# Kernel tuning notes

Hardware: AMD Instinct MI355X
Metric: run time of the kernel (lower is better)

## Reference

```python
import jax, jax.numpy as jnp
import numpy as np

NUM_EXPERTS = 8
TOP_K = 2
DIM = 1024
HIDDEN = 4096
BATCH, SEQ = 16, 32


def setup_inputs() -> dict:
    key = jax.random.key(0)
    k1, k2, k3, k4, k5 = jax.random.split(key, 5)
    scale = 1.0 / np.sqrt(DIM)
    return {
        "hidden_states": jax.random.normal(k1, (BATCH, SEQ, DIM), dtype=jnp.float32),
        "gate_w": jax.random.normal(k2, (NUM_EXPERTS, DIM), dtype=jnp.float32) * scale,
        "w1": jax.random.normal(k3, (NUM_EXPERTS, HIDDEN, DIM), dtype=jnp.float32) * scale,
        "w3": jax.random.normal(k4, (NUM_EXPERTS, HIDDEN, DIM), dtype=jnp.float32) * scale,
        "w2": jax.random.normal(k5, (NUM_EXPERTS, DIM, HIDDEN), dtype=jnp.float32) * (1.0 / np.sqrt(HIDDEN)),
    }


def reference(hidden_states, gate_w, w1, w3, w2):
    B, S, D = hidden_states.shape
    x = hidden_states.reshape(-1, D)  # [T, D]

    # Router: softmax in fp32, top-k, renormalize (Mixtral style)
    router_logits = x @ gate_w.T  # [T, E]
    probs = jax.nn.softmax(router_logits.astype(jnp.float32), axis=-1)
    routing_weights, selected_experts = jax.lax.top_k(probs, TOP_K)  # [T, K]
    routing_weights = routing_weights / routing_weights.sum(axis=-1, keepdims=True)
    routing_weights = routing_weights.astype(x.dtype)

    # Per-token per-expert combine coefficient: coef[t, e] = sum_k w[t,k] * 1[sel[t,k]==e]
    coef = (jax.nn.one_hot(selected_experts, NUM_EXPERTS, dtype=x.dtype)
            * routing_weights[..., None]).sum(axis=1)  # [T, E]

    # SwiGLU FFN for all experts (grouped GEMM form), combined by coef.
    h1 = jnp.einsum('td,ehd->teh', x, w1)           # [T, E, H]
    h3 = jnp.einsum('td,ehd->teh', x, w3)           # [T, E, H]
    act = jax.nn.silu(h1) * h3                      # [T, E, H]
    expert_out = jnp.einsum('teh,edh->ted', act, w2)  # [T, E, D]
    out = jnp.einsum('ted,te->td', expert_out, coef)  # [T, D]
    return out.reshape(B, S, D)
```

## Files before the change

kernel.cpp:

```cpp
#include <hip/hip_runtime.h>
#include <hip/hip_bf16.h>

#define E_ 8
#define D_ 1024
#define H_ 4096
#define T_ 512
#define A_ 1024
#define BM_ 192
#define NBUF 3

typedef __attribute__((ext_vector_type(8))) short bf16x8;
typedef __attribute__((ext_vector_type(4))) float f32x4;

__device__ __forceinline__ unsigned short f2bf(float f) {
  __hip_bfloat16 h = __float2bfloat16(f);
  return *reinterpret_cast<unsigned short*>(&h);
}

__device__ __forceinline__ bf16x8 pk8(float4 a, float4 b) {
  bf16x8 r;
  r[0] = (short)f2bf(a.x); r[1] = (short)f2bf(a.y);
  r[2] = (short)f2bf(a.z); r[3] = (short)f2bf(a.w);
  r[4] = (short)f2bf(b.x); r[5] = (short)f2bf(b.y);
  r[6] = (short)f2bf(b.z); r[7] = (short)f2bf(b.w);
  return r;
}

__device__ __forceinline__ void gl16(const void* g, void* l) {
  __builtin_amdgcn_global_load_lds(
      (const __attribute__((address_space(1))) unsigned int*)g,
      (__attribute__((address_space(3))) unsigned int*)l, 16, 0, 0);
}

__global__ void moe_router(const float* __restrict__ x,
                           const float* __restrict__ gw,
                           unsigned short* __restrict__ xb,
                           int* __restrict__ sel,
                           float* __restrict__ wtop) {
  const int t = blockIdx.x;
  const int lane = threadIdx.x;
  const float* xr = x + (size_t)t * D_;

  float4 xv[4];
#pragma unroll
  for (int i = 0; i < 4; ++i) xv[i] = *reinterpret_cast<const float4*>(xr + (i * 64 + lane) * 4);
#pragma unroll
  for (int i = 0; i < 4; ++i) {
    ushort4 u;
    u.x = f2bf(xv[i].x); u.y = f2bf(xv[i].y); u.z = f2bf(xv[i].z); u.w = f2bf(xv[i].w);
    *reinterpret_cast<ushort4*>(xb + (size_t)t * D_ + (i * 64 + lane) * 4) = u;
  }

  float lg[E_];
  for (int e = 0; e < E_; ++e) {
    const float* g = gw + (size_t)e * D_;
    float p = 0.f;
#pragma unroll
    for (int i = 0; i < 4; ++i) {
      float4 gv = *reinterpret_cast<const float4*>(g + (i * 64 + lane) * 4);
      p += xv[i].x * gv.x + xv[i].y * gv.y + xv[i].z * gv.z + xv[i].w * gv.w;
    }
#pragma unroll
    for (int off = 32; off; off >>= 1) p += __shfl_xor(p, off);
    lg[e] = p;
  }
  if (lane == 0) {
    float m = lg[0];
    for (int e = 1; e < E_; ++e) m = fmaxf(m, lg[e]);
    float pr[E_];
    float s = 0.f;
    for (int e = 0; e < E_; ++e) { pr[e] = __expf(lg[e] - m); s += pr[e]; }
    const float inv = 1.f / s;
    for (int e = 0; e < E_; ++e) pr[e] *= inv;
    float v0 = -1.f, v1 = -1.f; int i0 = 0, i1 = 0;
    for (int e = 0; e < E_; ++e) {
      float p = pr[e];
      if (p > v0)      { v1 = v0; i1 = i0; v0 = p; i0 = e; }
      else if (p > v1) { v1 = p; i1 = e; }
    }
    const float s2 = 1.f / (v0 + v1);
    sel[2 * t] = i0; sel[2 * t + 1] = i1;
    wtop[2 * t] = v0 * s2; wtop[2 * t + 1] = v1 * s2;
  }
}

__global__ void moe_compact(const int* __restrict__ sel,
                            const float* __restrict__ wtop,
                            int* __restrict__ counts,
                            int* __restrict__ offsets,
                            int* __restrict__ tok,
                            int* __restrict__ slotof,
                            float* __restrict__ coef) {
  const int tid = threadIdx.x;
  const int e = tid >> 6;
  const int lane = tid & 63;
  __shared__ int cnt[E_], offs[E_];

  int base = 0;
  for (int c = 0; c < T_ / 64; ++c) {
    const int t = c * 64 + lane;
    const bool f = (sel[2 * t] == e) || (sel[2 * t + 1] == e);
    base += __popcll(__ballot(f));
  }
  if (lane == 0) cnt[e] = base;
  __syncthreads();
  if (tid == 0) {
    int o = 0;
    for (int i = 0; i < E_; ++i) { offs[i] = o; o += cnt[i]; }
  }
  __syncthreads();
  if (lane == 0) { counts[e] = cnt[e]; offsets[e] = offs[e]; }

  int pos = offs[e];
  for (int c = 0; c < T_ / 64; ++c) {
    const int t = c * 64 + lane;
    const int s0 = sel[2 * t], s1 = sel[2 * t + 1];
    const bool f = (s0 == e) || (s1 == e);
    unsigned long long b = __ballot(f);
    const int myp = pos + __popcll(b & ((1ull << lane) - 1ull));
    if (f) {
      const int k = (s0 == e) ? 0 : 1;
      tok[myp] = t;
      slotof[2 * t + k] = myp;
      coef[myp] = wtop[2 * t + k];
    }
    pos += __popcll(b);
  }
}


#define WAITS(it, nit)                                                        \
    if ((it) == 0)              asm volatile("s_waitcnt vmcnt(4)" ::: "memory"); \
    else if ((it) == (nit) - 1) asm volatile("s_waitcnt vmcnt(3)" ::: "memory"); \
    else                        asm volatile("s_waitcnt vmcnt(7)" ::: "memory"); \
    __builtin_amdgcn_s_barrier();                                             \
    __builtin_amdgcn_sched_barrier(0);

#define STAGE1(s, kt) do {                                                    \
    gl16(b1src[0] + (kt), &B1s[s][wid * 256]);                                \
    gl16(b1src[1] + (kt), &B1s[s][1024 + wid * 256]);                         \
    gl16(b3src[0] + (kt), &B3s[s][wid * 256]);                                \
    gl16(b3src[1] + (kt), &B3s[s][1024 + wid * 256]);                         \
  } while (0)

__launch_bounds__(256, 3)
__global__ void moe_ffn1(const unsigned short* __restrict__ xb,
                         const float* __restrict__ w1,
                         const float* __restrict__ w3,
                         const int* __restrict__ counts,
                         const int* __restrict__ offsets,
                         const int* __restrict__ tok,
                         unsigned short* __restrict__ act) {
  const int bid = blockIdx.x;
  const int e = bid & 7;
  const int hg = bid >> 3;
  const int count = counts[e];
  const int off = offsets[e];
  const int hbase = hg * 64;

  __shared__ float B1s[NBUF][64 * 32];
  __shared__ float B3s[NBUF][64 * 32];

  const int tid = threadIdx.x;
  const int lane = tid & 63, wid = tid >> 6;
  const int lr = lane & 15, kg = lane >> 4;
  const int wm = wid * 48;

  const int cB = (((lane & 7) ^ (lane >> 3)) << 2);
  const float* b1src[2];
  const float* b3src[2];
#pragma unroll
  for (int j = 0; j < 2; ++j) {
    const int row = (j * 4 + wid) * 8 + (lane >> 3);
    b1src[j] = w1 + ((size_t)e * H_ + hbase + row) * D_ + cB;
    b3src[j] = w3 + ((size_t)e * H_ + hbase + row) * D_ + cB;
  }
  const int q0 = (((2 * kg) ^ (lr & 7)) << 2);
  const int q1 = (((2 * kg + 1) ^ (lr & 7)) << 2);

  for (int m0 = 0; m0 < count; m0 += BM_) {
    const unsigned short* ap[3];
#pragma unroll
    for (int mf = 0; mf < 3; ++mf) {
      const int row = m0 + wm + mf * 16 + lr;
      const int cr = (row < count) ? row : (count - 1);
      ap[mf] = xb + (size_t)tok[off + cr] * D_ + kg * 8;
    }
    const int qq = count - m0 - wm;
    const int mfn = (qq <= 0) ? 0 : ((qq + 15) >> 4 < 3 ? (qq + 15) >> 4 : 3);

    f32x4 acc1[3][4] = {};
    f32x4 acc3[3][4] = {};

    STAGE1(0, 0);
    STAGE1(1, 32);

    int cur = 0;
    for (int it = 0; it < 32; ++it) {
      WAITS(it, 32);

      bf16x8 af[3];
#pragma unroll
      for (int mf = 0; mf < 3; ++mf)
        af[mf] = *reinterpret_cast<const bf16x8*>(ap[mf] + it * 32);

      if (it + 2 < 32) {
        int s2 = cur + 2; if (s2 >= NBUF) s2 -= NBUF;
        STAGE1(s2, (it + 2) * 32);
      }

#pragma unroll
      for (int nf = 0; nf < 4; ++nf) {
        const int rb = (nf * 16 + lr) * 32;
        bf16x8 b1f = pk8(*reinterpret_cast<const float4*>(&B1s[cur][rb + q0]),
                         *reinterpret_cast<const float4*>(&B1s[cur][rb + q1]));
        bf16x8 b3f = pk8(*reinterpret_cast<const float4*>(&B3s[cur][rb + q0]),
                         *reinterpret_cast<const float4*>(&B3s[cur][rb + q1]));
#pragma unroll
        for (int mf = 0; mf < 3; ++mf)
          if (mf < mfn) {
            acc1[mf][nf] = __builtin_amdgcn_mfma_f32_16x16x32_bf16(af[mf], b1f, acc1[mf][nf], 0, 0, 0);
            acc3[mf][nf] = __builtin_amdgcn_mfma_f32_16x16x32_bf16(af[mf], b3f, acc3[mf][nf], 0, 0, 0);
          }
      }
      ++cur; if (cur >= NBUF) cur -= NBUF;
    }

#pragma unroll
    for (int mf = 0; mf < 3; ++mf) {
#pragma unroll
      for (int r = 0; r < 4; ++r) {
        const int mrow = m0 + wm + mf * 16 + kg * 4 + r;
        if (mrow < count) {
          const size_t rb = (size_t)(off + mrow) * H_;
#pragma unroll
          for (int nf = 0; nf < 4; ++nf) {
            const float h1 = acc1[mf][nf][r];
            const float h3 = acc3[mf][nf][r];
            const float a = h1 / (1.f + __expf(-h1)) * h3;
            act[rb + hbase + nf * 16 + lr] = f2bf(a);
          }
        }
      }
    }
    __syncthreads();
  }
}

#define STAGE2(s, kt) do {                                                    \
    gl16(bsrc[0] + (kt), &Bs[s][wid * 256]);                                  \
    gl16(bsrc[1] + (kt), &Bs[s][1024 + wid * 256]);                           \
  } while (0)

__launch_bounds__(256, 4)
__global__ void moe_ffn2(const unsigned short* __restrict__ act,
                         const float* __restrict__ w2,
                         const int* __restrict__ counts,
                         const int* __restrict__ offsets,
                         const float* __restrict__ coef,
                         float* __restrict__ part,
                         int kschunk) {
  const int bid = blockIdx.x;
  const int e = bid & 7;
  const int r2 = bid >> 3;
  const int dg = r2 & 15;
  const int ks = r2 >> 4;
  const int count = counts[e];
  const int off = offsets[e];
  const int dbase = dg * 64;
  const int kbase = ks * kschunk;
  const int nit = kschunk >> 5;

  __shared__ float Bs[NBUF][64 * 32];

  const int tid = threadIdx.x;
  const int lane = tid & 63, wid = tid >> 6;
  const int lr = lane & 15, kg = lane >> 4;
  const int wm = wid * 48;

  const int cB = (((lane & 7) ^ (lane >> 3)) << 2);
  const float* bsrc[2];
#pragma unroll
  for (int j = 0; j < 2; ++j) {
    const int row = (j * 4 + wid) * 8 + (lane >> 3);
    bsrc[j] = w2 + ((size_t)e * D_ + dbase + row) * H_ + kbase + cB;
  }
  const int q0 = (((2 * kg) ^ (lr & 7)) << 2);
  const int q1 = (((2 * kg + 1) ^ (lr & 7)) << 2);

  for (int m0 = 0; m0 < count; m0 += BM_) {
    const unsigned short* ap[3];
#pragma unroll
    for (int mf = 0; mf < 3; ++mf) {
      const int row = m0 + wm + mf * 16 + lr;
      const int cr = (row < count) ? row : (count - 1);
      ap[mf] = act + (size_t)(off + cr) * H_ + kbase + kg * 8;
    }
    const int qq = count - m0 - wm;
    const int mfn = (qq <= 0) ? 0 : ((qq + 15) >> 4 < 3 ? (qq + 15) >> 4 : 3);

    f32x4 acc[3][4] = {};

    STAGE2(0, 0);
    STAGE2(1, 32);

    int cur = 0;
    for (int it = 0; it < nit; ++it) {
      WAITS(it, nit);

      bf16x8 af[3];
#pragma unroll
      for (int mf = 0; mf < 3; ++mf)
        af[mf] = *reinterpret_cast<const bf16x8*>(ap[mf] + it * 32);

      if (it + 2 < nit) {
        int s2 = cur + 2; if (s2 >= NBUF) s2 -= NBUF;
        STAGE2(s2, (it + 2) * 32);
      }

#pragma unroll
      for (int nf = 0; nf < 4; ++nf) {
        const int rb = (nf * 16 + lr) * 32;
        bf16x8 bf = pk8(*reinterpret_cast<const float4*>(&Bs[cur][rb + q0]),
                        *reinterpret_cast<const float4*>(&Bs[cur][rb + q1]));
#pragma unroll
        for (int mf = 0; mf < 3; ++mf)
          if (mf < mfn)
            acc[mf][nf] = __builtin_amdgcn_mfma_f32_16x16x32_bf16(af[mf], bf, acc[mf][nf], 0, 0, 0);
      }
      ++cur; if (cur >= NBUF) cur -= NBUF;
    }

#pragma unroll
    for (int mf = 0; mf < 3; ++mf) {
#pragma unroll
      for (int r = 0; r < 4; ++r) {
        const int mrow = m0 + wm + mf * 16 + kg * 4 + r;
        if (mrow < count) {
          const float cf = coef[off + mrow];
          float* prow = part + ((size_t)ks * A_ + off + mrow) * D_;
#pragma unroll
          for (int nf = 0; nf < 4; ++nf)
            prow[dbase + nf * 16 + lr] = cf * acc[mf][nf][r];
        }
      }
    }
    __syncthreads();
  }
}

__global__ void moe_combine(const float* __restrict__ part,
                            const int* __restrict__ slotof,
                            float* __restrict__ out,
                            int ksn) {
  const int t = blockIdx.x;
  const int i = threadIdx.x;
  const int g0 = slotof[2 * t], g1 = slotof[2 * t + 1];
  float4 o = make_float4(0.f, 0.f, 0.f, 0.f);
  for (int ks = 0; ks < ksn; ++ks) {
    const float* p = part + (size_t)ks * A_ * D_;
    float4 a = reinterpret_cast<const float4*>(p + (size_t)g0 * D_)[i];
    float4 b = reinterpret_cast<const float4*>(p + (size_t)g1 * D_)[i];
    o.x += a.x + b.x; o.y += a.y + b.y; o.z += a.z + b.z; o.w += a.w + b.w;
  }
  reinterpret_cast<float4*>(out + (size_t)t * D_)[i] = o;
}

extern "C" void kernel_launch(void* const* d_in, const int* in_sizes, int n_in,
                              void* d_out, int out_size, void* d_ws, size_t ws_size,
                              hipStream_t stream) {
  const float* x  = (const float*)d_in[0];
  const float* gw = (const float*)d_in[1];
  const float* w1 = (const float*)d_in[2];
  const float* w3 = (const float*)d_in[3];
  const float* w2 = (const float*)d_in[4];
  float* out = (float*)d_out;

  char* ws = (char*)d_ws;
  const size_t SM   = 32768;
  const size_t ACT  = (size_t)A_ * H_ * 2;
  const size_t XB   = (size_t)T_ * D_ * 2;
  const size_t P1   = (size_t)A_ * D_ * 4;

  char* sm = ws;
  unsigned short* act = (unsigned short*)(ws + SM);
  unsigned short* xb  = (unsigned short*)(ws + SM + ACT);
  float* part         = (float*)(ws + SM + ACT + XB);
  const size_t base = SM + ACT + XB;
  const int ksn = (ws_size >= base + 8 * P1) ? 8 :
                  (ws_size >= base + 4 * P1) ? 4 :
                  (ws_size >= base + 2 * P1) ? 2 : 1;

  int*   sel     = (int*)  (sm);
  float* wtop    = (float*)(sm + 4096);
  int*   counts  = (int*)  (sm + 8192);
  int*   offsets = (int*)  (sm + 8192 + 64);
  int*   tokl    = (int*)  (sm + 12288);
  int*   slotof  = (int*)  (sm + 16384);
  float* coef    = (float*)(sm + 20480);

  moe_router <<<T_, 64, 0, stream>>>(x, gw, xb, sel, wtop);
  moe_compact<<<1, 512, 0, stream>>>(sel, wtop, counts, offsets, tokl, slotof, coef);
  moe_ffn1   <<<E_ * 64, 256, 0, stream>>>(xb, w1, w3, counts, offsets, tokl, act);
  moe_ffn2   <<<E_ * 16 * ksn, 256, 0, stream>>>(act, w2, counts, offsets, coef, part, H_ / ksn);
  moe_combine<<<T_, 256, 0, stream>>>(part, slotof, out, ksn);
}
```

Measured before the change: 143.3 us.

## Halve N tile, deepen LDS pipeline, double-buffer A fragments in expert GEMMs

Both expert GEMM kernels now use a 32-wide output tile instead of 64, which doubles the grid to 1024 blocks for ffn1 and 256*ksn for ffn2. The weight stream goes through a 4-deep LDS ring with prefetch distance three, and the loop is unrolled by two with even/odd A-fragment register sets so the activation loads for the next step overlap the current MFMAs. s_setprio is raised around the MFMA blocks, and ffn1 occupancy is raised to 4. The aim is more blocks in flight and better latency hiding for this weight-bandwidth-bound problem. In exchange, the A tile is reloaded from memory twice as often, and the hand-tuned vmcnt counts must match the new load counts exactly.

New measurement: 183.1 us. +27.8%, slower.

```diff
diff --git a/kernel.cpp b/kernel.cpp
--- a/kernel.cpp
+++ b/kernel.cpp
@@ -7,7 +7,7 @@
 #define T_ 512
 #define A_ 1024
 #define BM_ 192
-#define NBUF 3
+#define NBUF 4
 
 typedef __attribute__((ext_vector_type(8))) short bf16x8;
 typedef __attribute__((ext_vector_type(4))) float f32x4;
@@ -31,6 +31,12 @@
       (const __attribute__((address_space(1))) unsigned int*)g,
       (__attribute__((address_space(3))) unsigned int*)l, 16, 0, 0);
 }
+
+#define WV3 asm volatile("s_waitcnt vmcnt(3)" ::: "memory")
+#define WV4 asm volatile("s_waitcnt vmcnt(4)" ::: "memory")
+#define WV5 asm volatile("s_waitcnt vmcnt(5)" ::: "memory")
+#define WV0 asm volatile("s_waitcnt vmcnt(0)" ::: "memory")
+#define BARX do { __builtin_amdgcn_s_barrier(); __builtin_amdgcn_sched_barrier(0); } while (0)
 
 __global__ void moe_router(const float* __restrict__ x,
                            const float* __restrict__ gw,
@@ -129,21 +135,40 @@
 }
 
 
-#define WAITS(it, nit)                                                        \
-    if ((it) == 0)              asm volatile("s_waitcnt vmcnt(4)" ::: "memory"); \
-    else if ((it) == (nit) - 1) asm volatile("s_waitcnt vmcnt(3)" ::: "memory"); \
-    else                        asm volatile("s_waitcnt vmcnt(7)" ::: "memory"); \
-    __builtin_amdgcn_s_barrier();                                             \
-    __builtin_amdgcn_sched_barrier(0);
-
-#define STAGE1(s, kt) do {                                                    \
-    gl16(b1src[0] + (kt), &B1s[s][wid * 256]);                                \
-    gl16(b1src[1] + (kt), &B1s[s][1024 + wid * 256]);                         \
-    gl16(b3src[0] + (kt), &B3s[s][wid * 256]);                                \
-    gl16(b3src[1] + (kt), &B3s[s][1024 + wid * 256]);                         \
+#define STAGE1(S, KT)                                                        \
+  do {                                                                       \
+    gl16(b1p + (KT) * 32, B1s + (S) * 1024 + wid * 256);                     \
+    gl16(b3p + (KT) * 32, B3s + (S) * 1024 + wid * 256);                     \
   } while (0)
 
-__launch_bounds__(256, 3)
+#define LOADA1(SET, KA)                                                      \
+  do {                                                                       \
+    _Pragma("unroll")                                                        \
+    for (int mf = 0; mf < 3; ++mf)                                           \
+      SET[mf] = *reinterpret_cast<const bf16x8*>(ap[mf] + (KA) * 32);        \
+  } while (0)
+
+#define MFMA1(RD, ASET)                                                      \
+  do {                                                                       \
+    const float* bb1 = B1s + (RD) * 1024;                                    \
+    const float* bb3 = B3s + (RD) * 1024;                                    \
+    _Pragma("unroll")                                                        \
+    for (int nf = 0; nf < 2; ++nf) {                                         \
+      const int rb = (nf * 16 + lr) * 32;                                    \
+      bf16x8 b1f = pk8(*reinterpret_cast<const float4*>(bb1 + rb + q0),      \
+                       *reinterpret_cast<const float4*>(bb1 + rb + q1));     \
+      bf16x8 b3f = pk8(*reinterpret_cast<const float4*>(bb3 + rb + q0),      \
+                       *reinterpret_cast<const float4*>(bb3 + rb + q1));     \
+      _Pragma("unroll")                                                      \
+      for (int mf = 0; mf < 3; ++mf)                                         \
+        if (mf < mfn) {                                                      \
+          acc1[mf][nf] = __builtin_amdgcn_mfma_f32_16x16x32_bf16(ASET[mf], b1f, acc1[mf][nf], 0, 0, 0); \
+          acc3[mf][nf] = __builtin_amdgcn_mfma_f32_16x16x32_bf16(ASET[mf], b3f, acc3[mf][nf], 0, 0, 0); \
+        }                                                                    \
+    }                                                                        \
+  } while (0)
+
+__launch_bounds__(256, 4)
 __global__ void moe_ffn1(const unsigned short* __restrict__ xb,
                          const float* __restrict__ w1,
                          const float* __restrict__ w3,
@@ -156,10 +181,10 @@
   const int hg = bid >> 3;
   const int count = counts[e];
   const int off = offsets[e];
-  const int hbase = hg * 64;
-
-  __shared__ float B1s[NBUF][64 * 32];
-  __shared__ float B3s[NBUF][64 * 32];
+  const int hbase = hg * 32;
+
+  __shared__ float B1s[NBUF * 1024];
+  __shared__ float B3s[NBUF * 1024];
 
   const int tid = threadIdx.x;
   const int lane = tid & 63, wid = tid >> 6;
@@ -167,14 +192,8 @@
   const int wm = wid * 48;
 
   const int cB = (((lane & 7) ^ (lane >> 3)) << 2);
-  const float* b1src[2];
-  const float* b3src[2];
-#pragma unroll
-  for (int j = 0; j < 2; ++j) {
-    const int row = (j * 4 + wid) * 8 + (lane >> 3);
-    b1src[j] = w1 + ((size_t)e * H_ + hbase + row) * D_ + cB;
-    b3src[j] = w3 + ((size_t)e * H_ + hbase + row) * D_ + cB;
-  }
+  const float* b1p = w1 + ((size_t)e * H_ + hbase + wid * 8 + (lane >> 3)) * D_ + cB;
+  const float* b3p = w3 + ((size_t)e * H_ + hbase + wid * 8 + (lane >> 3)) * D_ + cB;
   const int q0 = (((2 * kg) ^ (lr & 7)) << 2);
   const int q1 = (((2 * kg + 1) ^ (lr & 7)) << 2);
 
@@ -189,41 +208,34 @@
     const int qq = count - m0 - wm;
     const int mfn = (qq <= 0) ? 0 : ((qq + 15) >> 4 < 3 ? (qq + 15) >> 4 : 3);
 
-    f32x4 acc1[3][4] = {};
-    f32x4 acc3[3][4] = {};
-
-    STAGE1(0, 0);
-    STAGE1(1, 32);
-
-    int cur = 0;
-    for (int it = 0; it < 32; ++it) {
-      WAITS(it, 32);
-
-      bf16x8 af[3];
-#pragma unroll
-      for (int mf = 0; mf < 3; ++mf)
-        af[mf] = *reinterpret_cast<const bf16x8*>(ap[mf] + it * 32);
-
-      if (it + 2 < 32) {
-        int s2 = cur + 2; if (s2 >= NBUF) s2 -= NBUF;
-        STAGE1(s2, (it + 2) * 32);
-      }
-
-#pragma unroll
-      for (int nf = 0; nf < 4; ++nf) {
-        const int rb = (nf * 16 + lr) * 32;
-        bf16x8 b1f = pk8(*reinterpret_cast<const float4*>(&B1s[cur][rb + q0]),
-                         *reinterpret_cast<const float4*>(&B1s[cur][rb + q1]));
-        bf16x8 b3f = pk8(*reinterpret_cast<const float4*>(&B3s[cur][rb + q0]),
-                         *reinterpret_cast<const float4*>(&B3s[cur][rb + q1]));
-#pragma unroll
-        for (int mf = 0; mf < 3; ++mf)
-          if (mf < mfn) {
-            acc1[mf][nf] = __builtin_amdgcn_mfma_f32_16x16x32_bf16(af[mf], b1f, acc1[mf][nf], 0, 0, 0);
-            acc3[mf][nf] = __builtin_amdgcn_mfma_f32_16x16x32_bf16(af[mf], b3f, acc3[mf][nf], 0, 0, 0);
-          }
-      }
-      ++cur; if (cur >= NBUF) cur -= NBUF;
+    f32x4 acc1[3][2] = {};
+    f32x4 acc3[3][2] = {};
+    bf16x8 aE[3], aO[3];
+
+    STAGE1(0, 0); STAGE1(1, 1); STAGE1(2, 2);
+    LOADA1(aE, 0); LOADA1(aO, 1);
+
+    int rd = 0;
+    for (int t = 0; t < 32; t += 2) {
+      if (t == 0) { WV3; } else { WV5; }
+      BARX;
+      { int s = rd + 3; if (s >= NBUF) s -= NBUF;
+        int kt = t + 3; if (kt > 31) kt = 31; STAGE1(s, kt); }
+      __builtin_amdgcn_s_setprio(1);
+      MFMA1(rd, aE);
+      __builtin_amdgcn_s_setprio(0);
+      { int ka = t + 2; if (ka > 31) ka = 31; LOADA1(aE, ka); }
+      ++rd; if (rd == NBUF) rd = 0;
+
+      WV5;
+      BARX;
+      { int s = rd + 3; if (s >= NBUF) s -= NBUF;
+        int kt = t + 4; if (kt > 31) kt = 31; STAGE1(s, kt); }
+      __builtin_amdgcn_s_setprio(1);
+      MFMA1(rd, aO);
+      __builtin_amdgcn_s_setprio(0);
+      { int ka = t + 3; if (ka > 31) ka = 31; LOADA1(aO, ka); }
+      ++rd; if (rd == NBUF) rd = 0;
     }
 
 #pragma unroll
@@ -234,7 +246,7 @@
         if (mrow < count) {
           const size_t rb = (size_t)(off + mrow) * H_;
 #pragma unroll
-          for (int nf = 0; nf < 4; ++nf) {
+          for (int nf = 0; nf < 2; ++nf) {
             const float h1 = acc1[mf][nf][r];
             const float h3 = acc3[mf][nf][r];
             const float a = h1 / (1.f + __expf(-h1)) * h3;
@@ -243,13 +255,33 @@
         }
       }
     }
+    WV0;
     __syncthreads();
   }
 }
 
-#define STAGE2(s, kt) do {                                                    \
-    gl16(bsrc[0] + (kt), &Bs[s][wid * 256]);                                  \
-    gl16(bsrc[1] + (kt), &Bs[s][1024 + wid * 256]);                           \
+#define STAGE2(S, KT) gl16(b2p + (KT) * 32, Bs + (S) * 1024 + wid * 256)
+
+#define LOADA2(SET, KA)                                                      \
+  do {                                                                       \
+    _Pragma("unroll")                                                        \
+    for (int mf = 0; mf < 3; ++mf)                                           \
+      SET[mf] = *reinterpret_cast<const bf16x8*>(ap[mf] + (KA) * 32);        \
+  } while (0)
+
+#define MFMA2(RD, ASET)                                                      \
+  do {                                                                       \
+    const float* bb = Bs + (RD) * 1024;                                      \
+    _Pragma("unroll")                                                        \
+    for (int nf = 0; nf < 2; ++nf) {                                         \
+      const int rb = (nf * 16 + lr) * 32;                                    \
+      bf16x8 bf = pk8(*reinterpret_cast<const float4*>(bb + rb + q0),        \
+                      *reinterpret_cast<const float4*>(bb + rb + q1));       \
+      _Pragma("unroll")                                                      \
+      for (int mf = 0; mf < 3; ++mf)                                         \
+        if (mf < mfn)                                                        \
+          acc[mf][nf] = __builtin_amdgcn_mfma_f32_16x16x32_bf16(ASET[mf], bf, acc[mf][nf], 0, 0, 0); \
+    }                                                                        \
   } while (0)
 
 __launch_bounds__(256, 4)
@@ -262,16 +294,16 @@
                          int kschunk) {
   const int bid = blockIdx.x;
   const int e = bid & 7;
-  const int r2 = bid >> 3;
-  const int dg = r2 & 15;
-  const int ks = r2 >> 4;
+  const int rest = bid >> 3;
+  const int dg = rest & 31;
+  const int ks = rest >> 5;
   const int count = counts[e];
   const int off = offsets[e];
-  const int dbase = dg * 64;
+  const int dbase = dg * 32;
   const int kbase = ks * kschunk;
   const int nit = kschunk >> 5;
 
-  __shared__ float Bs[NBUF][64 * 32];
+  __shared__ float Bs[NBUF * 1024];
 
   const int tid = threadIdx.x;
   const int lane = tid & 63, wid = tid >> 6;
@@ -279,12 +311,7 @@
   const int wm = wid * 48;
 
   const int cB = (((lane & 7) ^ (lane >> 3)) << 2);
-  const float* bsrc[2];
-#pragma unroll
-  for (int j = 0; j < 2; ++j) {
-    const int row = (j * 4 + wid) * 8 + (lane >> 3);
-    bsrc[j] = w2 + ((size_t)e * D_ + dbase + row) * H_ + kbase + cB;
-  }
+  const float* b2p = w2 + ((size_t)e * D_ + dbase + wid * 8 + (lane >> 3)) * H_ + kbase + cB;
   const int q0 = (((2 * kg) ^ (lr & 7)) << 2);
   const int q1 = (((2 * kg + 1) ^ (lr & 7)) << 2);
 
@@ -299,36 +326,34 @@
     const int qq = count - m0 - wm;
     const int mfn = (qq <= 0) ? 0 : ((qq + 15) >> 4 < 3 ? (qq + 15) >> 4 : 3);
 
-    f32x4 acc[3][4] = {};
-
-    STAGE2(0, 0);
-    STAGE2(1, 32);
-
-    int cur = 0;
-    for (int it = 0; it < nit; ++it) {
-      WAITS(it, nit);
-
-      bf16x8 af[3];
-#pragma unroll
-      for (int mf = 0; mf < 3; ++mf)
-        af[mf] = *reinterpret_cast<const bf16x8*>(ap[mf] + it * 32);
-
-      if (it + 2 < nit) {
-        int s2 = cur + 2; if (s2 >= NBUF) s2 -= NBUF;
-        STAGE2(s2, (it + 2) * 32);
-      }
-
-#pragma unroll
-      for (int nf = 0; nf < 4; ++nf) {
-        const int rb = (nf * 16 + lr) * 32;
-        bf16x8 bf = pk8(*reinterpret_cast<const float4*>(&Bs[cur][rb + q0]),
-                        *reinterpret_cast<const float4*>(&Bs[cur][rb + q1]));
-#pragma unroll
-        for (int mf = 0; mf < 3; ++mf)
-          if (mf < mfn)
-            acc[mf][nf] = __builtin_amdgcn_mfma_f32_16x16x32_bf16(af[mf], bf, acc[mf][nf], 0, 0, 0);
-      }
-      ++cur; if (cur >= NBUF) cur -= NBUF;
+    f32x4 acc[3][2] = {};
+    bf16x8 aE[3], aO[3];
+
+    STAGE2(0, 0); STAGE2(1, 1); STAGE2(2, 2);
+    LOADA2(aE, 0); LOADA2(aO, 1);
+
+    int rd = 0;
+    const int last = nit - 1;
+    for (int t = 0; t < nit; t += 2) {
+      if (t == 0) { WV3; } else { WV4; }
+      BARX;
+      { int s = rd + 3; if (s >= NBUF) s -= NBUF;
+        int kt = t + 3; if (kt > last) kt = last; STAGE2(s, kt); }
+      __builtin_amdgcn_s_setprio(1);
+      MFMA2(rd, aE);
+      __builtin_amdgcn_s_setprio(0);
+      { int ka = t + 2; if (ka > last) ka = last; LOADA2(aE, ka); }
+      ++rd; if (rd == NBUF) rd = 0;
+
+      WV4;
+      BARX;
+      { int s = rd + 3; if (s >= NBUF) s -= NBUF;
+        int kt = t + 4; if (kt > last) kt = last; STAGE2(s, kt); }
+      __builtin_amdgcn_s_setprio(1);
+      MFMA2(rd, aO);
+      __builtin_amdgcn_s_setprio(0);
+      { int ka = t + 3; if (ka > last) ka = last; LOADA2(aO, ka); }
+      ++rd; if (rd == NBUF) rd = 0;
     }
 
 #pragma unroll
@@ -340,11 +365,12 @@
           const float cf = coef[off + mrow];
           float* prow = part + ((size_t)ks * A_ + off + mrow) * D_;
 #pragma unroll
-          for (int nf = 0; nf < 4; ++nf)
+          for (int nf = 0; nf < 2; ++nf)
             prow[dbase + nf * 16 + lr] = cf * acc[mf][nf][r];
         }
       }
     }
+    WV0;
     __syncthreads();
   }
 }
@@ -401,7 +427,7 @@
 
   moe_router <<<T_, 64, 0, stream>>>(x, gw, xb, sel, wtop);
   moe_compact<<<1, 512, 0, stream>>>(sel, wtop, counts, offsets, tokl, slotof, coef);
-  moe_ffn1   <<<E_ * 64, 256, 0, stream>>>(xb, w1, w3, counts, offsets, tokl, act);
-  moe_ffn2   <<<E_ * 16 * ksn, 256, 0, stream>>>(act, w2, counts, offsets, coef, part, H_ / ksn);
+  moe_ffn1   <<<E_ * 128, 256, 0, stream>>>(xb, w1, w3, counts, offsets, tokl, act);
+  moe_ffn2   <<<E_ * 32 * ksn, 256, 0, stream>>>(act, w2, counts, offsets, coef, part, H_ / ksn);
   moe_combine<<<T_, 256, 0, stream>>>(part, slotof, out, ksn);
 }
```

## Double-buffer BK=64 K tiles and pre-gather routed tokens into contiguous bf16 buffer

Applied to the files above, without the earlier changes.

Both FFN GEMMs move from a 3-stage pipeline of 32-wide K tiles with fine-grained vmcnt waits to a 2-stage double buffer of 64-wide K tiles. Each stage drains all loads before a barrier and prefetches the next stage's A fragments into registers. A new gather kernel writes routed tokens into an expert-contiguous bf16 buffer, so FFN1 no longer does indirect token lookups. Occupancy hints drop to 2 blocks per CU, and blocks for empty experts return early. The full vmcnt(0) drain per stage may expose more memory latency than the earlier partial waits, and the extra launch adds overhead.

Measured after the change: 214.0 us. +49.4%, slower.

```diff
diff --git a/kernel.cpp b/kernel.cpp
--- a/kernel.cpp
+++ b/kernel.cpp
@@ -7,7 +7,7 @@
 #define T_ 512
 #define A_ 1024
 #define BM_ 192
-#define NBUF 3
+#define BK_ 64
 
 typedef __attribute__((ext_vector_type(8))) short bf16x8;
 typedef __attribute__((ext_vector_type(4))) float f32x4;
@@ -32,9 +32,14 @@
       (__attribute__((address_space(3))) unsigned int*)l, 16, 0, 0);
 }
 
+#define DRAIN_BAR do {                                         \
+    asm volatile("s_waitcnt vmcnt(0)" ::: "memory");           \
+    __builtin_amdgcn_s_barrier();                              \
+    __builtin_amdgcn_sched_barrier(0);                         \
+  } while (0)
+
 __global__ void moe_router(const float* __restrict__ x,
                            const float* __restrict__ gw,
-                           unsigned short* __restrict__ xb,
                            int* __restrict__ sel,
                            float* __restrict__ wtop) {
   const int t = blockIdx.x;
@@ -44,12 +49,6 @@
   float4 xv[4];
 #pragma unroll
   for (int i = 0; i < 4; ++i) xv[i] = *reinterpret_cast<const float4*>(xr + (i * 64 + lane) * 4);
-#pragma unroll
-  for (int i = 0; i < 4; ++i) {
-    ushort4 u;
-    u.x = f2bf(xv[i].x); u.y = f2bf(xv[i].y); u.z = f2bf(xv[i].z); u.w = f2bf(xv[i].w);
-    *reinterpret_cast<ushort4*>(xb + (size_t)t * D_ + (i * 64 + lane) * 4) = u;
-  }
 
   float lg[E_];
   for (int e = 0; e < E_; ++e) {
@@ -128,55 +127,93 @@
   }
 }
 
-
-#define WAITS(it, nit)                                                        \
-    if ((it) == 0)              asm volatile("s_waitcnt vmcnt(4)" ::: "memory"); \
-    else if ((it) == (nit) - 1) asm volatile("s_waitcnt vmcnt(3)" ::: "memory"); \
-    else                        asm volatile("s_waitcnt vmcnt(7)" ::: "memory"); \
-    __builtin_amdgcn_s_barrier();                                             \
-    __builtin_amdgcn_sched_barrier(0);
-
-#define STAGE1(s, kt) do {                                                    \
-    gl16(b1src[0] + (kt), &B1s[s][wid * 256]);                                \
-    gl16(b1src[1] + (kt), &B1s[s][1024 + wid * 256]);                         \
-    gl16(b3src[0] + (kt), &B3s[s][wid * 256]);                                \
-    gl16(b3src[1] + (kt), &B3s[s][1024 + wid * 256]);                         \
-  } while (0)
-
-__launch_bounds__(256, 3)
-__global__ void moe_ffn1(const unsigned short* __restrict__ xb,
+__global__ void moe_gather(const float* __restrict__ x,
+                           const int* __restrict__ tok,
+                           unsigned short* __restrict__ xc) {
+  const int slot = blockIdx.x;
+  const int i = threadIdx.x;
+  const int t = tok[slot];
+  float4 v = *reinterpret_cast<const float4*>(x + (size_t)t * D_ + i * 4);
+  ushort4 u;
+  u.x = f2bf(v.x); u.y = f2bf(v.y); u.z = f2bf(v.z); u.w = f2bf(v.w);
+  *reinterpret_cast<ushort4*>(xc + (size_t)slot * D_ + i * 4) = u;
+}
+
+
+
+#define STAGE1(S, KT)                                                         \
+  do {                                                                        \
+    _Pragma("unroll")                                                         \
+    for (int j = 0; j < 4; ++j) {                                             \
+      gl16(b1p[j] + (KT), &B1s[S][(wid * 4 + j) * 256]);                      \
+      gl16(b3p[j] + (KT), &B3s[S][(wid * 4 + j) * 256]);                      \
+    }                                                                         \
+  } while (0)
+
+#define LOADA1(SET, IT)                                                       \
+  do {                                                                        \
+    _Pragma("unroll")                                                         \
+    for (int mf = 0; mf < 3; ++mf) {                                          \
+      SET[mf * 2 + 0] = *reinterpret_cast<const bf16x8*>(ap[mf] + (IT) * 64); \
+      SET[mf * 2 + 1] = *reinterpret_cast<const bf16x8*>(ap[mf] + (IT) * 64 + 32); \
+    }                                                                         \
+  } while (0)
+
+#define MFMA1(S, ASET)                                                        \
+  do {                                                                        \
+    _Pragma("unroll")                                                         \
+    for (int ks = 0; ks < 2; ++ks) {                                          \
+      _Pragma("unroll")                                                       \
+      for (int nf = 0; nf < 4; ++nf) {                                        \
+        const int ix = nf * 1024 + (ks ? o1 : o0);                            \
+        bf16x8 b1f = pk8(*reinterpret_cast<const float4*>(&B1s[S][ix]),       \
+                         *reinterpret_cast<const float4*>(&B1s[S][ix + 4]));  \
+        bf16x8 b3f = pk8(*reinterpret_cast<const float4*>(&B3s[S][ix]),       \
+                         *reinterpret_cast<const float4*>(&B3s[S][ix + 4]));  \
+        _Pragma("unroll")                                                     \
+        for (int mf = 0; mf < 3; ++mf)                                        \
+          if (mf < mfn) {                                                     \
+            acc1[mf][nf] = __builtin_amdgcn_mfma_f32_16x16x32_bf16(ASET[mf * 2 + ks], b1f, acc1[mf][nf], 0, 0, 0); \
+            acc3[mf][nf] = __builtin_amdgcn_mfma_f32_16x16x32_bf16(ASET[mf * 2 + ks], b3f, acc3[mf][nf], 0, 0, 0); \
+          }                                                                   \
+      }                                                                       \
+    }                                                                         \
+  } while (0)
+
+__launch_bounds__(256, 2)
+__global__ void moe_ffn1(const unsigned short* __restrict__ xc,
                          const float* __restrict__ w1,
                          const float* __restrict__ w3,
                          const int* __restrict__ counts,
                          const int* __restrict__ offsets,
-                         const int* __restrict__ tok,
                          unsigned short* __restrict__ act) {
   const int bid = blockIdx.x;
   const int e = bid & 7;
   const int hg = bid >> 3;
   const int count = counts[e];
+  if (count <= 0) return;
   const int off = offsets[e];
   const int hbase = hg * 64;
 
-  __shared__ float B1s[NBUF][64 * 32];
-  __shared__ float B3s[NBUF][64 * 32];
+  __shared__ float B1s[2][64 * 64];
+  __shared__ float B3s[2][64 * 64];
 
   const int tid = threadIdx.x;
   const int lane = tid & 63, wid = tid >> 6;
   const int lr = lane & 15, kg = lane >> 4;
   const int wm = wid * 48;
 
-  const int cB = (((lane & 7) ^ (lane >> 3)) << 2);
-  const float* b1src[2];
-  const float* b3src[2];
-#pragma unroll
-  for (int j = 0; j < 2; ++j) {
-    const int row = (j * 4 + wid) * 8 + (lane >> 3);
-    b1src[j] = w1 + ((size_t)e * H_ + hbase + row) * D_ + cB;
-    b3src[j] = w3 + ((size_t)e * H_ + hbase + row) * D_ + cB;
-  }
-  const int q0 = (((2 * kg) ^ (lr & 7)) << 2);
-  const int q1 = (((2 * kg + 1) ^ (lr & 7)) << 2);
+  const float* b1p[4];
+  const float* b3p[4];
+#pragma unroll
+  for (int j = 0; j < 4; ++j) {
+    const int R = (wid * 4 + j) * 4 + (lane >> 4);
+    const int sc = ((lane & 15) ^ (R & 6)) << 2;
+    b1p[j] = w1 + ((size_t)e * H_ + hbase + R) * D_ + sc;
+    b3p[j] = w3 + ((size_t)e * H_ + hbase + R) * D_ + sc;
+  }
+  const int o0 = lr * 64 + (((kg * 2) ^ (lr & 6)) << 2);
+  const int o1 = lr * 64 + (((8 + kg * 2) ^ (lr & 6)) << 2);
 
   for (int m0 = 0; m0 < count; m0 += BM_) {
     const unsigned short* ap[3];
@@ -184,46 +221,25 @@
     for (int mf = 0; mf < 3; ++mf) {
       const int row = m0 + wm + mf * 16 + lr;
       const int cr = (row < count) ? row : (count - 1);
-      ap[mf] = xb + (size_t)tok[off + cr] * D_ + kg * 8;
+      ap[mf] = xc + (size_t)(off + cr) * D_ + kg * 8;
     }
     const int qq = count - m0 - wm;
     const int mfn = (qq <= 0) ? 0 : ((qq + 15) >> 4 < 3 ? (qq + 15) >> 4 : 3);
 
     f32x4 acc1[3][4] = {};
     f32x4 acc3[3][4] = {};
+    bf16x8 aE[6], aO[6];
 
     STAGE1(0, 0);
-    STAGE1(1, 32);
-
-    int cur = 0;
-    for (int it = 0; it < 32; ++it) {
-      WAITS(it, 32);
-
-      bf16x8 af[3];
-#pragma unroll
-      for (int mf = 0; mf < 3; ++mf)
-        af[mf] = *reinterpret_cast<const bf16x8*>(ap[mf] + it * 32);
-
-      if (it + 2 < 32) {
-        int s2 = cur + 2; if (s2 >= NBUF) s2 -= NBUF;
-        STAGE1(s2, (it + 2) * 32);
-      }
-
-#pragma unroll
-      for (int nf = 0; nf < 4; ++nf) {
-        const int rb = (nf * 16 + lr) * 32;
-        bf16x8 b1f = pk8(*reinterpret_cast<const float4*>(&B1s[cur][rb + q0]),
-                         *reinterpret_cast<const float4*>(&B1s[cur][rb + q1]));
-        bf16x8 b3f = pk8(*reinterpret_cast<const float4*>(&B3s[cur][rb + q0]),
-                         *reinterpret_cast<const float4*>(&B3s[cur][rb + q1]));
-#pragma unroll
-        for (int mf = 0; mf < 3; ++mf)
-          if (mf < mfn) {
-            acc1[mf][nf] = __builtin_amdgcn_mfma_f32_16x16x32_bf16(af[mf], b1f, acc1[mf][nf], 0, 0, 0);
-            acc3[mf][nf] = __builtin_amdgcn_mfma_f32_16x16x32_bf16(af[mf], b3f, acc3[mf][nf], 0, 0, 0);
-          }
-      }
-      ++cur; if (cur >= NBUF) cur -= NBUF;
+    LOADA1(aE, 0);
+
+    for (int it = 0; it < 16; it += 2) {
+      DRAIN_BAR;
+      if (it + 1 < 16) { STAGE1(1, (it + 1) * BK_); LOADA1(aO, it + 1); }
+      MFMA1(0, aE);
+      DRAIN_BAR;
+      if (it + 2 < 16) { STAGE1(0, (it + 2) * BK_); LOADA1(aE, it + 2); }
+      MFMA1(1, aO);
     }
 
 #pragma unroll
@@ -247,12 +263,31 @@
   }
 }
 
-#define STAGE2(s, kt) do {                                                    \
-    gl16(bsrc[0] + (kt), &Bs[s][wid * 256]);                                  \
-    gl16(bsrc[1] + (kt), &Bs[s][1024 + wid * 256]);                           \
-  } while (0)
-
-__launch_bounds__(256, 4)
+#define STAGE2(S, KT)                                                         \
+  do {                                                                        \
+    _Pragma("unroll")                                                         \
+    for (int j = 0; j < 4; ++j)                                               \
+      gl16(b2p[j] + (KT), &Bs[S][(wid * 4 + j) * 256]);                       \
+  } while (0)
+
+#define MFMA2(S, ASET)                                                        \
+  do {                                                                        \
+    _Pragma("unroll")                                                         \
+    for (int ks = 0; ks < 2; ++ks) {                                          \
+      _Pragma("unroll")                                                       \
+      for (int nf = 0; nf < 4; ++nf) {                                        \
+        const int ix = nf * 1024 + (ks ? o1 : o0);                            \
+        bf16x8 bf = pk8(*reinterpret_cast<const float4*>(&Bs[S][ix]),         \
+                        *reinterpret_cast<const float4*>(&Bs[S][ix + 4]));    \
+        _Pragma("unroll")                                                     \
+        for (int mf = 0; mf < 3; ++mf)                                        \
+          if (mf < mfn)                                                       \
+            acc[mf][nf] = __builtin_amdgcn_mfma_f32_16x16x32_bf16(ASET[mf * 2 + ks], bf, acc[mf][nf], 0, 0, 0); \
+      }                                                                       \
+    }                                                                         \
+  } while (0)
+
+__launch_bounds__(256, 2)
 __global__ void moe_ffn2(const unsigned short* __restrict__ act,
                          const float* __restrict__ w2,
                          const int* __restrict__ counts,
@@ -262,31 +297,32 @@
                          int kschunk) {
   const int bid = blockIdx.x;
   const int e = bid & 7;
-  const int r2 = bid >> 3;
-  const int dg = r2 & 15;
-  const int ks = r2 >> 4;
+  const int rest = bid >> 3;
+  const int dg = rest & 15;
+  const int ks0 = rest >> 4;
   const int count = counts[e];
+  if (count <= 0) return;
   const int off = offsets[e];
   const int dbase = dg * 64;
-  const int kbase = ks * kschunk;
-  const int nit = kschunk >> 5;
-
-  __shared__ float Bs[NBUF][64 * 32];
+  const int kbase = ks0 * kschunk;
+  const int nit = kschunk >> 6;
+
+  __shared__ float Bs[2][64 * 64];
 
   const int tid = threadIdx.x;
   const int lane = tid & 63, wid = tid >> 6;
   const int lr = lane & 15, kg = lane >> 4;
   const int wm = wid * 48;
 
-  const int cB = (((lane & 7) ^ (lane >> 3)) << 2);
-  const float* bsrc[2];
-#pragma unroll
-  for (int j = 0; j < 2; ++j) {
-    const int row = (j * 4 + wid) * 8 + (lane >> 3);
-    bsrc[j] = w2 + ((size_t)e * D_ + dbase + row) * H_ + kbase + cB;
-  }
-  const int q0 = (((2 * kg) ^ (lr & 7)) << 2);
-  const int q1 = (((2 * kg + 1) ^ (lr & 7)) << 2);
+  const float* b2p[4];
+#pragma unroll
+  for (int j = 0; j < 4; ++j) {
+    const int R = (wid * 4 + j) * 4 + (lane >> 4);
+    const int sc = ((lane & 15) ^ (R & 6)) << 2;
+    b2p[j] = w2 + ((size_t)e * D_ + dbase + R) * H_ + kbase + sc;
+  }
+  const int o0 = lr * 64 + (((kg * 2) ^ (lr & 6)) << 2);
+  const int o1 = lr * 64 + (((8 + kg * 2) ^ (lr & 6)) << 2);
 
   for (int m0 = 0; m0 < count; m0 += BM_) {
     const unsigned short* ap[3];
@@ -300,35 +336,18 @@
     const int mfn = (qq <= 0) ? 0 : ((qq + 15) >> 4 < 3 ? (qq + 15) >> 4 : 3);
 
     f32x4 acc[3][4] = {};
+    bf16x8 aE[6], aO[6];
 
     STAGE2(0, 0);
-    STAGE2(1, 32);
-
-    int cur = 0;
-    for (int it = 0; it < nit; ++it) {
-      WAITS(it, nit);
-
-      bf16x8 af[3];
-#pragma unroll
-      for (int mf = 0; mf < 3; ++mf)
-        af[mf] = *reinterpret_cast<const bf16x8*>(ap[mf] + it * 32);
-
-      if (it + 2 < nit) {
-        int s2 = cur + 2; if (s2 >= NBUF) s2 -= NBUF;
-        STAGE2(s2, (it + 2) * 32);
-      }
-
-#pragma unroll
-      for (int nf = 0; nf < 4; ++nf) {
-        const int rb = (nf * 16 + lr) * 32;
-        bf16x8 bf = pk8(*reinterpret_cast<const float4*>(&Bs[cur][rb + q0]),
-                        *reinterpret_cast<const float4*>(&Bs[cur][rb + q1]));
-#pragma unroll
-        for (int mf = 0; mf < 3; ++mf)
-          if (mf < mfn)
-            acc[mf][nf] = __builtin_amdgcn_mfma_f32_16x16x32_bf16(af[mf], bf, acc[mf][nf], 0, 0, 0);
-      }
-      ++cur; if (cur >= NBUF) cur -= NBUF;
+    LOADA1(aE, 0);
+
+    for (int it = 0; it < nit; it += 2) {
+      DRAIN_BAR;
+      if (it + 1 < nit) { STAGE2(1, (it + 1) * BK_); LOADA1(aO, it + 1); }
+      MFMA2(0, aE);
+      DRAIN_BAR;
+      if (it + 2 < nit) { STAGE2(0, (it + 2) * BK_); LOADA1(aE, it + 2); }
+      MFMA2(1, aO);
     }
 
 #pragma unroll
@@ -338,7 +357,7 @@
         const int mrow = m0 + wm + mf * 16 + kg * 4 + r;
         if (mrow < count) {
           const float cf = coef[off + mrow];
-          float* prow = part + ((size_t)ks * A_ + off + mrow) * D_;
+          float* prow = part + ((size_t)ks0 * A_ + off + mrow) * D_;
 #pragma unroll
           for (int nf = 0; nf < 4; ++nf)
             prow[dbase + nf * 16 + lr] = cf * acc[mf][nf][r];
@@ -377,16 +396,16 @@
   float* out = (float*)d_out;
 
   char* ws = (char*)d_ws;
-  const size_t SM   = 32768;
-  const size_t ACT  = (size_t)A_ * H_ * 2;
-  const size_t XB   = (size_t)T_ * D_ * 2;
-  const size_t P1   = (size_t)A_ * D_ * 4;
+  const size_t SM  = 32768;
+  const size_t XC  = (size_t)A_ * D_ * 2;
+  const size_t ACT = (size_t)A_ * H_ * 2;
+  const size_t P1  = (size_t)A_ * D_ * 4;
 
   char* sm = ws;
-  unsigned short* act = (unsigned short*)(ws + SM);
-  unsigned short* xb  = (unsigned short*)(ws + SM + ACT);
-  float* part         = (float*)(ws + SM + ACT + XB);
-  const size_t base = SM + ACT + XB;
+  unsigned short* xc  = (unsigned short*)(ws + SM);
+  unsigned short* act = (unsigned short*)(ws + SM + XC);
+  float* part         = (float*)(ws + SM + XC + ACT);
+  const size_t base = SM + XC + ACT;
   const int ksn = (ws_size >= base + 8 * P1) ? 8 :
                   (ws_size >= base + 4 * P1) ? 4 :
                   (ws_size >= base + 2 * P1) ? 2 : 1;
@@ -399,9 +418,10 @@
   int*   slotof  = (int*)  (sm + 16384);
   float* coef    = (float*)(sm + 20480);
 
-  moe_router <<<T_, 64, 0, stream>>>(x, gw, xb, sel, wtop);
+  moe_router <<<T_, 64, 0, stream>>>(x, gw, sel, wtop);
   moe_compact<<<1, 512, 0, stream>>>(sel, wtop, counts, offsets, tokl, slotof, coef);
-  moe_ffn1   <<<E_ * 64, 256, 0, stream>>>(xb, w1, w3, counts, offsets, tokl, act);
+  moe_gather <<<A_, 256, 0, stream>>>(x, tokl, xc);
+  moe_ffn1   <<<E_ * 64, 256, 0, stream>>>(xc, w1, w3, counts, offsets, act);
   moe_ffn2   <<<E_ * 16 * ksn, 256, 0, stream>>>(act, w2, counts, offsets, coef, part, H_ / ksn);
   moe_combine<<<T_, 256, 0, stream>>>(part, slotof, out, ksn);
 }
```
